# Kernel tuning notes

Measured on AMD Instinct MI355X. Metric: run time of the kernel, lower is better.

## Reference

```python
import jax, jax.numpy as jnp
import numpy as np

D_IN = 1024
D_OUT = 1024
SEQ = 2048
BATCH = 4


def setup_inputs() -> dict:
    key = jax.random.key(0)
    kx, kq, kk, kv = jax.random.split(key, 4)
    x = jax.random.normal(kx, (BATCH, SEQ, D_IN), dtype=jnp.float32)
    s = 1.0 / np.sqrt(D_IN)
    Wq = jax.random.uniform(kq, (D_IN, D_OUT), dtype=jnp.float32, minval=-s, maxval=s)
    Wk = jax.random.uniform(kk, (D_IN, D_OUT), dtype=jnp.float32, minval=-s, maxval=s)
    Wv = jax.random.uniform(kv, (D_IN, D_OUT), dtype=jnp.float32, minval=-s, maxval=s)
    return {"x": x, "Wq": Wq, "Wk": Wk, "Wv": Wv}


def reference(x, Wq, Wk, Wv):
    d_k = Wq.shape[1]
    q = jnp.einsum('bsd,de->bse', x, Wq)
    k = jnp.einsum('bsd,de->bse', x, Wk)
    v = jnp.einsum('bsd,de->bse', x, Wv)
    # [B, S, S] raw scores
    scores = jnp.einsum('bqe,bke->bqk', q, k)
    S = scores.shape[-1]
    causal = jnp.triu(jnp.ones((S, S), dtype=bool), k=1)  # True above diagonal
    scores = jnp.where(causal, -jnp.inf, scores)
    attn = jax.nn.softmax(scores * (d_k ** -0.5), axis=-1)
    # dropout p=0.0 -> identity
    return jnp.einsum('bqk,bke->bqe', attn, v)
```

## Files before the change

### kernel.cpp

```cpp
#include <hip/hip_runtime.h>
#include <hip/hip_bf16.h>

typedef unsigned short u16;
typedef __bf16 bfx8 __attribute__((ext_vector_type(8)));
typedef float fx4 __attribute__((ext_vector_type(4)));

#define SEQ 2048
#define DIM 1024
#define NBATCH 4
#define SCALE 0.03125f
#define NEL ((size_t)NBATCH * SEQ * DIM)

__device__ inline u16 f2bf(float f) {
    __bf16 h = (__bf16)f;
    return __builtin_bit_cast(unsigned short, h);
}

#define GLL(gp, lp) __builtin_amdgcn_global_load_lds( \
    (const __attribute__((address_space(1))) unsigned int*)(gp), \
    (__attribute__((address_space(3))) unsigned int*)(lp), 16, 0, 0)

__global__ __launch_bounds__(256) void prep(
    const float* __restrict__ X,
    const float* __restrict__ Wq, const float* __restrict__ Wk,
    const float* __restrict__ Wv,
    u16* __restrict__ XB, u16* __restrict__ WT, float* __restrict__ Lrow)
{
    __shared__ u16 t[32][33];
    int bid = blockIdx.x;
    int tid = threadIdx.x;
    if (bid < 8192) {
        size_t i = (size_t)bid * 256 + tid;
        float4 v = ((const float4*)X)[i];
        uint2 pk;
        pk.x = (unsigned)f2bf(v.x) | ((unsigned)f2bf(v.y) << 16);
        pk.y = (unsigned)f2bf(v.z) | ((unsigned)f2bf(v.w) << 16);
        ((uint2*)XB)[i] = pk;
    } else if (bid < 11264) {
        int tt = bid - 8192;
        int z = tt >> 10, t2 = tt & 1023;
        const float* W = (z == 0) ? Wq : (z == 1) ? Wk : Wv;
        u16* out = WT + (size_t)z * 1024 * 1024;
        int n0 = (t2 & 31) * 32, k0 = (t2 >> 5) * 32;
        int tx = tid & 31, ty = tid >> 5;
        #pragma unroll
        for (int i = 0; i < 32; i += 8)
            t[ty + i][tx] = f2bf(W[(size_t)(k0 + ty + i) * 1024 + n0 + tx]);
        __syncthreads();
        #pragma unroll
        for (int i = 0; i < 32; i += 8)
            out[(size_t)(n0 + ty + i) * 1024 + k0 + tx] = t[tx][ty + i];
    } else {
        int i = (bid - 11264) * 256 + tid;
        Lrow[i] = 0.0f;
    }
}

__global__ __launch_bounds__(256) void gemm_fast(
    const u16* __restrict__ XB, const u16* __restrict__ WT,
    u16* __restrict__ Qo, u16* __restrict__ Ko, u16* __restrict__ VTo)
{
    const u16* Wz = WT + (size_t)blockIdx.z * 1024 * 1024;
    int m0 = blockIdx.y * 128, n0 = blockIdx.x * 128;

    __shared__ __align__(16) u16 As[128 * 32];
    __shared__ __align__(16) u16 Bs[128 * 32];
    __shared__ __align__(16) u16 Ct[64][132];

    int tid = threadIdx.x, lane = tid & 63, w = tid >> 6;
    int wm = w >> 1, wn = w & 1, lo = lane & 15, qd = lane >> 4;

    fx4 acc[4][4] = {};

    int c0 = tid, c1 = tid + 256;
    const u16* a0 = XB + (size_t)(m0 + (c0 >> 2)) * 1024 + (c0 & 3) * 8;
    const u16* a1 = XB + (size_t)(m0 + (c1 >> 2)) * 1024 + (c1 & 3) * 8;
    const u16* b0 = Wz + (size_t)(n0 + (c0 >> 2)) * 1024 + (c0 & 3) * 8;
    const u16* b1 = Wz + (size_t)(n0 + (c1 >> 2)) * 1024 + (c1 & 3) * 8;

    for (int k0 = 0; k0 < 1024; k0 += 32) {
        GLL(a0 + k0, &As[(size_t)c0 * 8]);
        GLL(a1 + k0, &As[(size_t)c1 * 8]);
        GLL(b0 + k0, &Bs[(size_t)c0 * 8]);
        GLL(b1 + k0, &Bs[(size_t)c1 * 8]);
        __syncthreads();

        bfx8 af[4], bf[4];
        #pragma unroll
        for (int i = 0; i < 4; i++)
            af[i] = *(const bfx8*)(&As[(wm * 64 + i * 16 + lo) * 32 + qd * 8]);
        #pragma unroll
        for (int j = 0; j < 4; j++)
            bf[j] = *(const bfx8*)(&Bs[(wn * 64 + j * 16 + lo) * 32 + qd * 8]);
        #pragma unroll
        for (int i = 0; i < 4; i++)
            #pragma unroll
            for (int j = 0; j < 4; j++)
                acc[i][j] = __builtin_amdgcn_mfma_f32_16x16x32_bf16(af[i], bf[j], acc[i][j], 0, 0, 0);
        __syncthreads();
    }

    if (blockIdx.z != 2) {
        u16* C = (blockIdx.z == 0) ? Qo : Ko;
        #pragma unroll
        for (int i = 0; i < 4; i++)
            #pragma unroll
            for (int j = 0; j < 4; j++)
                #pragma unroll
                for (int r = 0; r < 4; r++) {
                    int row = m0 + wm * 64 + i * 16 + qd * 4 + r;
                    int col = n0 + wn * 64 + j * 16 + lo;
                    C[(size_t)row * 1024 + col] = f2bf(acc[i][j][r]);
                }
    } else {
        #pragma unroll
        for (int half = 0; half < 2; half++) {
            __syncthreads();
            if (wm == half) {
                #pragma unroll
                for (int i = 0; i < 4; i++)
                    #pragma unroll
                    for (int j = 0; j < 4; j++)
                        #pragma unroll
                        for (int r = 0; r < 4; r++)
                            Ct[i * 16 + qd * 4 + r][wn * 64 + j * 16 + lo] = f2bf(acc[i][j][r]);
            }
            __syncthreads();
            #pragma unroll
            for (int e = tid; e < 64 * 128; e += 256) {
                int d = e >> 6, sl = e & 63;
                int gr = m0 + half * 64 + sl;
                int bb = gr >> 11, s = gr & 2047;
                VTo[((size_t)bb * DIM + (n0 + d)) * SEQ + s] = Ct[sl][d];
            }
        }
    }
}

__global__ __launch_bounds__(256) void gemm_legacy(
    const float* __restrict__ X,
    const float* __restrict__ Wq, const float* __restrict__ Wk, const float* __restrict__ Wv,
    u16* __restrict__ Qo, u16* __restrict__ Ko, u16* __restrict__ VTo)
{
    const int K = 1024, N = 1024;
    const float* W = (blockIdx.z == 0) ? Wq : (blockIdx.z == 1) ? Wk : Wv;
    int m0 = blockIdx.y * 128, n0 = blockIdx.x * 128;
    __shared__ __align__(16) u16 As[128 * 40];
    __shared__ __align__(16) u16 Bs[128 * 40];
    __shared__ __align__(16) u16 Ct[64][132];
    int tid = threadIdx.x, lane = tid & 63, w = tid >> 6;
    int wm = w >> 1, wn = w & 1, lo = lane & 15, qd = lane >> 4;
    fx4 acc[4][4] = {};
    for (int k0 = 0; k0 < K; k0 += 32) {
        #pragma unroll
        for (int c = tid; c < 1024; c += 256) {
            int row = c >> 3, cc = (c & 7) * 4;
            float4 v = *(const float4*)(X + (size_t)(m0 + row) * K + k0 + cc);
            uint2 pk;
            pk.x = (unsigned)f2bf(v.x) | ((unsigned)f2bf(v.y) << 16);
            pk.y = (unsigned)f2bf(v.z) | ((unsigned)f2bf(v.w) << 16);
            *(uint2*)(&As[row * 40 + cc]) = pk;
        }
        #pragma unroll
        for (int c = tid; c < 1024; c += 256) {
            int r = c >> 5, cc = (c & 31) * 4;
            float4 v = *(const float4*)(W + (size_t)(k0 + r) * N + n0 + cc);
            Bs[(cc + 0) * 40 + r] = f2bf(v.x);
            Bs[(cc + 1) * 40 + r] = f2bf(v.y);
            Bs[(cc + 2) * 40 + r] = f2bf(v.z);
            Bs[(cc + 3) * 40 + r] = f2bf(v.w);
        }
        __syncthreads();
        bfx8 af[4], bf[4];
        #pragma unroll
        for (int i = 0; i < 4; i++)
            af[i] = *(const bfx8*)(&As[(wm * 64 + i * 16 + lo) * 40 + qd * 8]);
        #pragma unroll
        for (int j = 0; j < 4; j++)
            bf[j] = *(const bfx8*)(&Bs[(wn * 64 + j * 16 + lo) * 40 + qd * 8]);
        #pragma unroll
        for (int i = 0; i < 4; i++)
            #pragma unroll
            for (int j = 0; j < 4; j++)
                acc[i][j] = __builtin_amdgcn_mfma_f32_16x16x32_bf16(af[i], bf[j], acc[i][j], 0, 0, 0);
        __syncthreads();
    }
    if (blockIdx.z != 2) {
        u16* C = (blockIdx.z == 0) ? Qo : Ko;
        #pragma unroll
        for (int i = 0; i < 4; i++)
            #pragma unroll
            for (int j = 0; j < 4; j++)
                #pragma unroll
                for (int r = 0; r < 4; r++) {
                    int row = m0 + wm * 64 + i * 16 + qd * 4 + r;
                    int col = n0 + wn * 64 + j * 16 + lo;
                    C[(size_t)row * N + col] = f2bf(acc[i][j][r]);
                }
    } else {
        #pragma unroll
        for (int half = 0; half < 2; half++) {
            __syncthreads();
            if (wm == half) {
                #pragma unroll
                for (int i = 0; i < 4; i++)
                    #pragma unroll
                    for (int j = 0; j < 4; j++)
                        #pragma unroll
                        for (int r = 0; r < 4; r++)
                            Ct[i * 16 + qd * 4 + r][wn * 64 + j * 16 + lo] = f2bf(acc[i][j][r]);
            }
            __syncthreads();
            #pragma unroll
            for (int e = tid; e < 64 * 128; e += 256) {
                int d = e >> 6, sl = e & 63;
                int gr = m0 + half * 64 + sl;
                int bb = gr >> 11, s = gr & 2047;
                VTo[((size_t)bb * DIM + (n0 + d)) * SEQ + s] = Ct[sl][d];
            }
        }
    }
}

__global__ __launch_bounds__(512) void sgemm_exp(
    const u16* __restrict__ Q, const u16* __restrict__ K,
    u16* __restrict__ P, float* __restrict__ Lrow)
{
    int b = blockIdx.y;
    int t = blockIdx.x;
    int i = (int)((sqrtf(8.0f * t + 1.0f) - 1.0f) * 0.5f);
    while ((i + 1) * (i + 2) / 2 <= t) i++;
    while (i * (i + 1) / 2 > t) i--;
    int j = t - i * (i + 1) / 2;

    const u16* Qb = Q + (size_t)b * SEQ * DIM;
    const u16* Kb = K + (size_t)b * SEQ * DIM;
    u16* Pb = P + (size_t)b * SEQ * SEQ;
    float* Lb = Lrow + (size_t)b * SEQ;

    int m0 = i * 128, n0 = j * 128;

    __shared__ __align__(16) u16 As[128 * 32];
    __shared__ __align__(16) u16 Bs[128 * 32];

    int tid = threadIdx.x, lane = tid & 63, w = tid >> 6;
    int wm = w >> 2, wn = w & 3, lo = lane & 15, qd = lane >> 4;

    fx4 acc[4][2] = {};

    int c0 = tid;
    const u16* a0 = Qb + (size_t)(m0 + (c0 >> 2)) * DIM + (c0 & 3) * 8;
    const u16* b0 = Kb + (size_t)(n0 + (c0 >> 2)) * DIM + (c0 & 3) * 8;

    for (int k0 = 0; k0 < 1024; k0 += 32) {
        GLL(a0 + k0, &As[(size_t)c0 * 8]);
        GLL(b0 + k0, &Bs[(size_t)c0 * 8]);
        __syncthreads();

        bfx8 af[4], bf[2];
        #pragma unroll
        for (int ii = 0; ii < 4; ii++)
            af[ii] = *(const bfx8*)(&As[(wm * 64 + ii * 16 + lo) * 32 + qd * 8]);
        #pragma unroll
        for (int jn = 0; jn < 2; jn++)
            bf[jn] = *(const bfx8*)(&Bs[(wn * 32 + jn * 16 + lo) * 32 + qd * 8]);
        #pragma unroll
        for (int ii = 0; ii < 4; ii++)
            #pragma unroll
            for (int jn = 0; jn < 2; jn++)
                acc[ii][jn] = __builtin_amdgcn_mfma_f32_16x16x32_bf16(af[ii], bf[jn], acc[ii][jn], 0, 0, 0);
        __syncthreads();
    }

    #pragma unroll
    for (int ii = 0; ii < 4; ii++)
        #pragma unroll
        for (int r = 0; r < 4; r++) {
            int row = m0 + wm * 64 + ii * 16 + qd * 4 + r;
            float rs = 0.0f;
            #pragma unroll
            for (int jn = 0; jn < 2; jn++) {
                int col = n0 + wn * 32 + jn * 16 + lo;
                float s = acc[ii][jn][r] * SCALE;
                s = fminf(fmaxf(s, -30.0f), 30.0f);
                float p = (col > row) ? 0.0f : __expf(s);
                Pb[(size_t)row * SEQ + col] = f2bf(p);
                rs += p;
            }
            #pragma unroll
            for (int off = 1; off < 16; off <<= 1) rs += __shfl_xor(rs, off);
            if (lo == 0) atomicAdd(&Lb[row], rs);
        }
}

__global__ __launch_bounds__(512) void pvgemm(
    const u16* __restrict__ P, const u16* __restrict__ VT,
    const float* __restrict__ Lrow, float* __restrict__ O)
{
    int b = blockIdx.y;
    int qb = 15 - (int)(blockIdx.x >> 3);
    int db = blockIdx.x & 7;
    int m0 = qb * 128, n0 = db * 128;
    int kext = (qb + 1) * 128;

    const u16* Pb = P + (size_t)b * SEQ * SEQ;
    const u16* Vb = VT + (size_t)b * DIM * SEQ;
    const float* Lb = Lrow + (size_t)b * SEQ;
    float* Ob = O + (size_t)b * SEQ * DIM;

    __shared__ __align__(16) u16 As[128 * 32];
    __shared__ __align__(16) u16 Bs[128 * 32];

    int tid = threadIdx.x, lane = tid & 63, w = tid >> 6;
    int wm = w >> 2, wn = w & 3, lo = lane & 15, qd = lane >> 4;

    fx4 acc[4][2] = {};

    int c0 = tid;
    const u16* a0 = Pb + (size_t)(m0 + (c0 >> 2)) * SEQ + (c0 & 3) * 8;
    const u16* b0 = Vb + (size_t)(n0 + (c0 >> 2)) * SEQ + (c0 & 3) * 8;

    for (int k0 = 0; k0 < kext; k0 += 32) {
        GLL(a0 + k0, &As[(size_t)c0 * 8]);
        GLL(b0 + k0, &Bs[(size_t)c0 * 8]);
        __syncthreads();

        bfx8 af[4], bf[2];
        #pragma unroll
        for (int ii = 0; ii < 4; ii++)
            af[ii] = *(const bfx8*)(&As[(wm * 64 + ii * 16 + lo) * 32 + qd * 8]);
        #pragma unroll
        for (int jn = 0; jn < 2; jn++)
            bf[jn] = *(const bfx8*)(&Bs[(wn * 32 + jn * 16 + lo) * 32 + qd * 8]);
        #pragma unroll
        for (int ii = 0; ii < 4; ii++)
            #pragma unroll
            for (int jn = 0; jn < 2; jn++)
                acc[ii][jn] = __builtin_amdgcn_mfma_f32_16x16x32_bf16(af[ii], bf[jn], acc[ii][jn], 0, 0, 0);
        __syncthreads();
    }

    #pragma unroll
    for (int ii = 0; ii < 4; ii++)
        #pragma unroll
        for (int r = 0; r < 4; r++) {
            int row = m0 + wm * 64 + ii * 16 + qd * 4 + r;
            float linv = 1.0f / Lb[row];
            #pragma unroll
            for (int jn = 0; jn < 2; jn++) {
                int col = n0 + wn * 32 + jn * 16 + lo;
                Ob[(size_t)row * DIM + col] = acc[ii][jn][r] * linv;
            }
        }
}

__global__ __launch_bounds__(512) void flash_attn(
    const u16* __restrict__ Q, const u16* __restrict__ Kmat,
    const u16* __restrict__ VT, float* __restrict__ O)
{
    int b = blockIdx.y;
    int qt = (int)(gridDim.x - 1) - (int)blockIdx.x;
    int q0 = qt * 32;
    int tid = threadIdx.x;
    int lane = tid & 63, w = tid >> 6;
    int lo = lane & 15, qd = lane >> 4;

    __shared__ __align__(16) float Sp[8][32][33];
    __shared__ __align__(16) __bf16 Pl[32][40];
    __shared__ float ml[32], ll[32], al[32];

    const u16* Qb = Q + (size_t)b * SEQ * DIM;
    const u16* Kb = Kmat + (size_t)b * SEQ * DIM;
    const u16* VTb = VT + (size_t)b * DIM * SEQ;

    bfx8 qf[2][4];
    #pragma unroll
    for (int i = 0; i < 2; i++)
        #pragma unroll
        for (int c = 0; c < 4; c++)
            qf[i][c] = *(const bfx8*)(Qb + (size_t)(q0 + i * 16 + lo) * DIM + w * 128 + c * 32 + qd * 8);

    fx4 oacc[2][8] = {};
    if (tid < 32) { ml[tid] = -INFINITY; ll[tid] = 0.0f; }
    __syncthreads();

    for (int kt = 0; kt <= qt; kt++) {
        int k0 = kt * 32;
        fx4 sp[2][2] = {};
        #pragma unroll
        for (int c = 0; c < 4; c++) {
            bfx8 kf[2];
            #pragma unroll
            for (int jn = 0; jn < 2; jn++)
                kf[jn] = *(const bfx8*)(Kb + (size_t)(k0 + jn * 16 + lo) * DIM + w * 128 + c * 32 + qd * 8);
            #pragma unroll
            for (int i = 0; i < 2; i++)
                #pragma unroll
                for (int jn = 0; jn < 2; jn++)
                    sp[i][jn] = __builtin_amdgcn_mfma_f32_16x16x32_bf16(qf[i][c], kf[jn], sp[i][jn], 0, 0, 0);
        }
        #pragma unroll
        for (int i = 0; i < 2; i++)
            #pragma unroll
            for (int jn = 0; jn < 2; jn++)
                #pragma unroll
                for (int r = 0; r < 4; r++)
                    Sp[w][i * 16 + qd * 4 + r][jn * 16 + lo] = sp[i][jn][r];
        __syncthreads();
        {
            int r = tid >> 4, ci = tid & 15;
            int q = q0 + r;
            float s0 = 0.0f, s1 = 0.0f;
            #pragma unroll
            for (int p = 0; p < 8; p++) { s0 += Sp[p][r][ci]; s1 += Sp[p][r][ci + 16]; }
            s0 = fminf(fmaxf(s0 * SCALE, -1e30f), 1e30f);
            s1 = fminf(fmaxf(s1 * SCALE, -1e30f), 1e30f);
            if (k0 + ci > q)      s0 = -INFINITY;
            if (k0 + ci + 16 > q) s1 = -INFINITY;
            float mx = fmaxf(s0, s1);
            #pragma unroll
            for (int off = 1; off < 16; off <<= 1) mx = fmaxf(mx, __shfl_xor(mx, off));
            float mo = ml[r];
            float mn = fmaxf(mo, mx);
            float p0 = __expf(s0 - mn), p1 = __expf(s1 - mn);
            Pl[r][ci] = (__bf16)p0;
            Pl[r][ci + 16] = (__bf16)p1;
            float ps = p0 + p1;
            #pragma unroll
            for (int off = 1; off < 16; off <<= 1) ps += __shfl_xor(ps, off);
            if (ci == 0) {
                float alpha = __expf(mo - mn);
                ll[r] = alpha * ll[r] + ps;
                ml[r] = mn;
                al[r] = alpha;
            }
        }
        __syncthreads();
        float alocal[2][4];
        #pragma unroll
        for (int i = 0; i < 2; i++)
            #pragma unroll
            for (int r = 0; r < 4; r++)
                alocal[i][r] = al[i * 16 + qd * 4 + r];
        #pragma unroll
        for (int i = 0; i < 2; i++)
            #pragma unroll
            for (int j = 0; j < 8; j++)
                #pragma unroll
                for (int r = 0; r < 4; r++)
                    oacc[i][j][r] *= alocal[i][r];
        bfx8 pf[2];
        #pragma unroll
        for (int i = 0; i < 2; i++)
            pf[i] = *(const bfx8*)(&Pl[i * 16 + lo][qd * 8]);
        #pragma unroll
        for (int j = 0; j < 8; j++) {
            bfx8 vf = *(const bfx8*)(VTb + (size_t)(w * 128 + j * 16 + lo) * SEQ + k0 + qd * 8);
            #pragma unroll
            for (int i = 0; i < 2; i++)
                oacc[i][j] = __builtin_amdgcn_mfma_f32_16x16x32_bf16(pf[i], vf, oacc[i][j], 0, 0, 0);
        }
    }

    float linv[2][4];
    #pragma unroll
    for (int i = 0; i < 2; i++)
        #pragma unroll
        for (int r = 0; r < 4; r++)
            linv[i][r] = 1.0f / ll[i * 16 + qd * 4 + r];
    float* Ob = O + (size_t)b * SEQ * DIM;
    #pragma unroll
    for (int i = 0; i < 2; i++)
        #pragma unroll
        for (int j = 0; j < 8; j++)
            #pragma unroll
            for (int r = 0; r < 4; r++) {
                int row = q0 + i * 16 + qd * 4 + r;
                int col = w * 128 + j * 16 + lo;
                Ob[(size_t)row * DIM + col] = oacc[i][j][r] * linv[i][r];
            }
}

extern "C" void kernel_launch(void* const* d_in, const int* in_sizes, int n_in,
                              void* d_out, int out_size, void* d_ws, size_t ws_size,
                              hipStream_t stream) {
    const float* x  = (const float*)d_in[0];
    const float* Wq = (const float*)d_in[1];
    const float* Wk = (const float*)d_in[2];
    const float* Wv = (const float*)d_in[3];

    u16* ws = (u16*)d_ws;
    u16* Qp  = ws;
    u16* Kp  = Qp + NEL;
    u16* VTp = Kp + NEL;
    u16* XBp = VTp + NEL;
    u16* WTp = XBp + NEL;
    u16*   Pm   = VTp + NEL;
    float* Lrow = (float*)(Pm + (size_t)NBATCH * SEQ * SEQ);

    size_t need_base = 3 * NEL * 2;
    size_t need_conv = NEL * 2 + (size_t)3 * 1024 * 1024 * 2;
    size_t need_mat  = (size_t)NBATCH * SEQ * SEQ * 2
                     + (size_t)NBATCH * SEQ * 4 + 1024;
    bool fastg = ws_size >= need_base + need_conv;
    bool mat   = ws_size >= need_base + need_mat;

    if (fastg && mat) {
        prep<<<dim3(11296), 256, 0, stream>>>(x, Wq, Wk, Wv, XBp, WTp, Lrow);
        gemm_fast<<<dim3(8, 64, 3), 256, 0, stream>>>(XBp, WTp, Qp, Kp, VTp);
        sgemm_exp<<<dim3(136, NBATCH), 512, 0, stream>>>(Qp, Kp, Pm, Lrow);
        pvgemm<<<dim3(128, NBATCH), 512, 0, stream>>>(Pm, VTp, Lrow, (float*)d_out);
    } else {
        gemm_legacy<<<dim3(8, 64, 3), 256, 0, stream>>>(x, Wq, Wk, Wv, Qp, Kp, VTp);
        flash_attn<<<dim3(SEQ / 32, NBATCH), 512, 0, stream>>>(
            Qp, Kp, VTp, (float*)d_out);
    }
}
```

Before: 255.1 us.

## Fold Wq·Wkᵀ into one matrix, swizzle LDS, and widen K-tiles

```diff
diff --git a/kernel.cpp b/kernel.cpp
--- a/kernel.cpp
+++ b/kernel.cpp
@@ -24,7 +24,8 @@
     const float* __restrict__ X,
     const float* __restrict__ Wq, const float* __restrict__ Wk,
     const float* __restrict__ Wv,
-    u16* __restrict__ XB, u16* __restrict__ WT, float* __restrict__ Lrow)
+    u16* __restrict__ XB, u16* __restrict__ WB, u16* __restrict__ WTv,
+    float* __restrict__ Lrow)
 {
     __shared__ u16 t[32][33];
     int bid = blockIdx.x;
@@ -36,62 +37,63 @@
         pk.x = (unsigned)f2bf(v.x) | ((unsigned)f2bf(v.y) << 16);
         pk.y = (unsigned)f2bf(v.z) | ((unsigned)f2bf(v.w) << 16);
         ((uint2*)XB)[i] = pk;
+    } else if (bid < 10240) {
+        int b2 = bid - 8192;
+        const float* W = (b2 < 1024) ? Wq : Wk;
+        u16* out = WB + (size_t)(b2 >> 10) * 1024 * 1024;
+        size_t i = (size_t)(b2 & 1023) * 256 + tid;
+        float4 v = ((const float4*)W)[i];
+        uint2 pk;
+        pk.x = (unsigned)f2bf(v.x) | ((unsigned)f2bf(v.y) << 16);
+        pk.y = (unsigned)f2bf(v.z) | ((unsigned)f2bf(v.w) << 16);
+        ((uint2*)out)[i] = pk;
     } else if (bid < 11264) {
-        int tt = bid - 8192;
-        int z = tt >> 10, t2 = tt & 1023;
-        const float* W = (z == 0) ? Wq : (z == 1) ? Wk : Wv;
-        u16* out = WT + (size_t)z * 1024 * 1024;
+        int t2 = bid - 10240;
         int n0 = (t2 & 31) * 32, k0 = (t2 >> 5) * 32;
         int tx = tid & 31, ty = tid >> 5;
         #pragma unroll
         for (int i = 0; i < 32; i += 8)
-            t[ty + i][tx] = f2bf(W[(size_t)(k0 + ty + i) * 1024 + n0 + tx]);
+            t[ty + i][tx] = f2bf(Wv[(size_t)(k0 + ty + i) * 1024 + n0 + tx]);
         __syncthreads();
         #pragma unroll
         for (int i = 0; i < 32; i += 8)
-            out[(size_t)(n0 + ty + i) * 1024 + k0 + tx] = t[tx][ty + i];
+            WTv[(size_t)(n0 + ty + i) * 1024 + k0 + tx] = t[tx][ty + i];
     } else {
         int i = (bid - 11264) * 256 + tid;
         Lrow[i] = 0.0f;
     }
 }
 
-__global__ __launch_bounds__(256) void gemm_fast(
-    const u16* __restrict__ XB, const u16* __restrict__ WT,
-    u16* __restrict__ Qo, u16* __restrict__ Ko, u16* __restrict__ VTo)
-{
-    const u16* Wz = WT + (size_t)blockIdx.z * 1024 * 1024;
+__global__ __launch_bounds__(256) void gemm_m(
+    const u16* __restrict__ WBk, const u16* __restrict__ WBq, u16* __restrict__ MT)
+{
     int m0 = blockIdx.y * 128, n0 = blockIdx.x * 128;
-
     __shared__ __align__(16) u16 As[128 * 32];
     __shared__ __align__(16) u16 Bs[128 * 32];
-    __shared__ __align__(16) u16 Ct[64][132];
-
     int tid = threadIdx.x, lane = tid & 63, w = tid >> 6;
     int wm = w >> 1, wn = w & 1, lo = lane & 15, qd = lane >> 4;
-
     fx4 acc[4][4] = {};
 
     int c0 = tid, c1 = tid + 256;
-    const u16* a0 = XB + (size_t)(m0 + (c0 >> 2)) * 1024 + (c0 & 3) * 8;
-    const u16* a1 = XB + (size_t)(m0 + (c1 >> 2)) * 1024 + (c1 & 3) * 8;
-    const u16* b0 = Wz + (size_t)(n0 + (c0 >> 2)) * 1024 + (c0 & 3) * 8;
-    const u16* b1 = Wz + (size_t)(n0 + (c1 >> 2)) * 1024 + (c1 & 3) * 8;
-
+    const u16* a0 = WBk + (size_t)(m0 + (c0 >> 2)) * 1024 + (((c0 & 3) ^ ((c0 >> 2) & 3)) * 8);
+    const u16* a1 = WBk + (size_t)(m0 + (c1 >> 2)) * 1024 + (((c1 & 3) ^ ((c1 >> 2) & 3)) * 8);
+    const u16* b0 = WBq + (size_t)(n0 + (c0 >> 2)) * 1024 + (((c0 & 3) ^ ((c0 >> 2) & 3)) * 8);
+    const u16* b1 = WBq + (size_t)(n0 + (c1 >> 2)) * 1024 + (((c1 & 3) ^ ((c1 >> 2) & 3)) * 8);
+
+    int sw = (qd ^ (lo & 3)) * 8;
     for (int k0 = 0; k0 < 1024; k0 += 32) {
         GLL(a0 + k0, &As[(size_t)c0 * 8]);
         GLL(a1 + k0, &As[(size_t)c1 * 8]);
         GLL(b0 + k0, &Bs[(size_t)c0 * 8]);
         GLL(b1 + k0, &Bs[(size_t)c1 * 8]);
         __syncthreads();
-
         bfx8 af[4], bf[4];
         #pragma unroll
         for (int i = 0; i < 4; i++)
-            af[i] = *(const bfx8*)(&As[(wm * 64 + i * 16 + lo) * 32 + qd * 8]);
+            af[i] = *(const bfx8*)(&As[(wm * 64 + i * 16 + lo) * 32 + sw]);
         #pragma unroll
         for (int j = 0; j < 4; j++)
-            bf[j] = *(const bfx8*)(&Bs[(wn * 64 + j * 16 + lo) * 32 + qd * 8]);
+            bf[j] = *(const bfx8*)(&Bs[(wn * 64 + j * 16 + lo) * 32 + sw]);
         #pragma unroll
         for (int i = 0; i < 4; i++)
             #pragma unroll
@@ -99,9 +101,63 @@
                 acc[i][j] = __builtin_amdgcn_mfma_f32_16x16x32_bf16(af[i], bf[j], acc[i][j], 0, 0, 0);
         __syncthreads();
     }
-
-    if (blockIdx.z != 2) {
-        u16* C = (blockIdx.z == 0) ? Qo : Ko;
+    #pragma unroll
+    for (int i = 0; i < 4; i++)
+        #pragma unroll
+        for (int j = 0; j < 4; j++)
+            #pragma unroll
+            for (int r = 0; r < 4; r++)
+                MT[(size_t)(m0 + wm * 64 + i * 16 + qd * 4 + r) * 1024
+                   + n0 + wn * 64 + j * 16 + lo] = f2bf(acc[i][j][r]);
+}
+
+__global__ __launch_bounds__(256) void gemm_fast(
+    const u16* __restrict__ XB, const u16* __restrict__ MT,
+    const u16* __restrict__ WTv,
+    u16* __restrict__ Yo, u16* __restrict__ VTo)
+{
+    const u16* Wz = (blockIdx.z == 0) ? MT : WTv;
+    int m0 = blockIdx.y * 128, n0 = blockIdx.x * 128;
+
+    __shared__ __align__(16) u16 As[128 * 32];
+    __shared__ __align__(16) u16 Bs[128 * 32];
+    __shared__ __align__(16) u16 Ct[64][132];
+
+    int tid = threadIdx.x, lane = tid & 63, w = tid >> 6;
+    int wm = w >> 1, wn = w & 1, lo = lane & 15, qd = lane >> 4;
+
+    fx4 acc[4][4] = {};
+
+    int c0 = tid, c1 = tid + 256;
+    const u16* a0 = XB + (size_t)(m0 + (c0 >> 2)) * 1024 + (((c0 & 3) ^ ((c0 >> 2) & 3)) * 8);
+    const u16* a1 = XB + (size_t)(m0 + (c1 >> 2)) * 1024 + (((c1 & 3) ^ ((c1 >> 2) & 3)) * 8);
+    const u16* b0 = Wz + (size_t)(n0 + (c0 >> 2)) * 1024 + (((c0 & 3) ^ ((c0 >> 2) & 3)) * 8);
+    const u16* b1 = Wz + (size_t)(n0 + (c1 >> 2)) * 1024 + (((c1 & 3) ^ ((c1 >> 2) & 3)) * 8);
+
+    int sw = (qd ^ (lo & 3)) * 8;
+    for (int k0 = 0; k0 < 1024; k0 += 32) {
+        GLL(a0 + k0, &As[(size_t)c0 * 8]);
+        GLL(a1 + k0, &As[(size_t)c1 * 8]);
+        GLL(b0 + k0, &Bs[(size_t)c0 * 8]);
+        GLL(b1 + k0, &Bs[(size_t)c1 * 8]);
+        __syncthreads();
+
+        bfx8 af[4], bf[4];
+        #pragma unroll
+        for (int i = 0; i < 4; i++)
+            af[i] = *(const bfx8*)(&As[(wm * 64 + i * 16 + lo) * 32 + sw]);
+        #pragma unroll
+        for (int j = 0; j < 4; j++)
+            bf[j] = *(const bfx8*)(&Bs[(wn * 64 + j * 16 + lo) * 32 + sw]);
+        #pragma unroll
+        for (int i = 0; i < 4; i++)
+            #pragma unroll
+            for (int j = 0; j < 4; j++)
+                acc[i][j] = __builtin_amdgcn_mfma_f32_16x16x32_bf16(af[i], bf[j], acc[i][j], 0, 0, 0);
+        __syncthreads();
+    }
+
+    if (blockIdx.z == 0) {
         #pragma unroll
         for (int i = 0; i < 4; i++)
             #pragma unroll
@@ -110,7 +166,7 @@
                 for (int r = 0; r < 4; r++) {
                     int row = m0 + wm * 64 + i * 16 + qd * 4 + r;
                     int col = n0 + wn * 64 + j * 16 + lo;
-                    C[(size_t)row * 1024 + col] = f2bf(acc[i][j][r]);
+                    Yo[(size_t)row * 1024 + col] = f2bf(acc[i][j][r]);
                 }
     } else {
         #pragma unroll
@@ -135,6 +191,154 @@
             }
         }
     }
+}
+
+__global__ __launch_bounds__(512) void sgemm_exp(
+    const u16* __restrict__ Y, const u16* __restrict__ XB,
+    u16* __restrict__ P, float* __restrict__ Lrow)
+{
+    int b = blockIdx.y;
+    int t = blockIdx.x;
+    int i = (int)((sqrtf(8.0f * t + 1.0f) - 1.0f) * 0.5f);
+    while ((i + 1) * (i + 2) / 2 <= t) i++;
+    while (i * (i + 1) / 2 > t) i--;
+    int j = t - i * (i + 1) / 2;
+
+    const u16* Yb = Y + (size_t)b * SEQ * DIM;
+    const u16* Xb = XB + (size_t)b * SEQ * DIM;
+    u16* Pb = P + (size_t)b * SEQ * SEQ;
+    float* Lb = Lrow + (size_t)b * SEQ;
+
+    int m0 = i * 128, n0 = j * 128;
+
+    __shared__ __align__(16) u16 As[128 * 64];
+    __shared__ __align__(16) u16 Bs[128 * 64];
+
+    int tid = threadIdx.x, lane = tid & 63, w = tid >> 6;
+    int wm = w >> 2, wn = w & 3, lo = lane & 15, qd = lane >> 4;
+
+    fx4 acc[4][2] = {};
+
+    int c0 = tid, c1 = tid + 512;
+    const u16* a0 = Yb + (size_t)(m0 + (c0 >> 3)) * 1024 + (((c0 & 7) ^ ((c0 >> 3) & 7)) * 8);
+    const u16* a1 = Yb + (size_t)(m0 + (c1 >> 3)) * 1024 + (((c1 & 7) ^ ((c1 >> 3) & 7)) * 8);
+    const u16* b0 = Xb + (size_t)(n0 + (c0 >> 3)) * 1024 + (((c0 & 7) ^ ((c0 >> 3) & 7)) * 8);
+    const u16* b1 = Xb + (size_t)(n0 + (c1 >> 3)) * 1024 + (((c1 & 7) ^ ((c1 >> 3) & 7)) * 8);
+
+    for (int k0 = 0; k0 < 1024; k0 += 64) {
+        GLL(a0 + k0, &As[(size_t)c0 * 8]);
+        GLL(a1 + k0, &As[(size_t)c1 * 8]);
+        GLL(b0 + k0, &Bs[(size_t)c0 * 8]);
+        GLL(b1 + k0, &Bs[(size_t)c1 * 8]);
+        __syncthreads();
+
+        #pragma unroll
+        for (int kc = 0; kc < 2; kc++) {
+            int sw = ((kc * 4 + qd) ^ (lo & 7)) * 8;
+            bfx8 af[4], bf[2];
+            #pragma unroll
+            for (int ii = 0; ii < 4; ii++)
+                af[ii] = *(const bfx8*)(&As[(wm * 64 + ii * 16 + lo) * 64 + sw]);
+            #pragma unroll
+            for (int jn = 0; jn < 2; jn++)
+                bf[jn] = *(const bfx8*)(&Bs[(wn * 32 + jn * 16 + lo) * 64 + sw]);
+            #pragma unroll
+            for (int ii = 0; ii < 4; ii++)
+                #pragma unroll
+                for (int jn = 0; jn < 2; jn++)
+                    acc[ii][jn] = __builtin_amdgcn_mfma_f32_16x16x32_bf16(af[ii], bf[jn], acc[ii][jn], 0, 0, 0);
+        }
+        __syncthreads();
+    }
+
+    #pragma unroll
+    for (int ii = 0; ii < 4; ii++)
+        #pragma unroll
+        for (int r = 0; r < 4; r++) {
+            int row = m0 + wm * 64 + ii * 16 + qd * 4 + r;
+            float rs = 0.0f;
+            #pragma unroll
+            for (int jn = 0; jn < 2; jn++) {
+                int col = n0 + wn * 32 + jn * 16 + lo;
+                float s = acc[ii][jn][r] * SCALE;
+                s = fminf(fmaxf(s, -30.0f), 30.0f);
+                float p = (col > row) ? 0.0f : __expf(s);
+                Pb[(size_t)row * SEQ + col] = f2bf(p);
+                rs += p;
+            }
+            #pragma unroll
+            for (int off = 1; off < 16; off <<= 1) rs += __shfl_xor(rs, off);
+            if (lo == 0) atomicAdd(&Lb[row], rs);
+        }
+}
+
+__global__ __launch_bounds__(512) void pvgemm(
+    const u16* __restrict__ P, const u16* __restrict__ VT,
+    const float* __restrict__ Lrow, float* __restrict__ O)
+{
+    int b = blockIdx.y;
+    int qb = 15 - (int)(blockIdx.x >> 3);
+    int db = blockIdx.x & 7;
+    int m0 = qb * 128, n0 = db * 128;
+    int kext = (qb + 1) * 128;
+
+    const u16* Pb = P + (size_t)b * SEQ * SEQ;
+    const u16* Vb = VT + (size_t)b * DIM * SEQ;
+    const float* Lb = Lrow + (size_t)b * SEQ;
+    float* Ob = O + (size_t)b * SEQ * DIM;
+
+    __shared__ __align__(16) u16 As[128 * 64];
+    __shared__ __align__(16) u16 Bs[128 * 64];
+
+    int tid = threadIdx.x, lane = tid & 63, w = tid >> 6;
+    int wm = w >> 2, wn = w & 3, lo = lane & 15, qd = lane >> 4;
+
+    fx4 acc[4][2] = {};
+
+    int c0 = tid, c1 = tid + 512;
+    const u16* a0 = Pb + (size_t)(m0 + (c0 >> 3)) * SEQ + (((c0 & 7) ^ ((c0 >> 3) & 7)) * 8);
+    const u16* a1 = Pb + (size_t)(m0 + (c1 >> 3)) * SEQ + (((c1 & 7) ^ ((c1 >> 3) & 7)) * 8);
+    const u16* b0 = Vb + (size_t)(n0 + (c0 >> 3)) * SEQ + (((c0 & 7) ^ ((c0 >> 3) & 7)) * 8);
+    const u16* b1 = Vb + (size_t)(n0 + (c1 >> 3)) * SEQ + (((c1 & 7) ^ ((c1 >> 3) & 7)) * 8);
+
+    for (int k0 = 0; k0 < kext; k0 += 64) {
+        GLL(a0 + k0, &As[(size_t)c0 * 8]);
+        GLL(a1 + k0, &As[(size_t)c1 * 8]);
+        GLL(b0 + k0, &Bs[(size_t)c0 * 8]);
+        GLL(b1 + k0, &Bs[(size_t)c1 * 8]);
+        __syncthreads();
+
+        #pragma unroll
+        for (int kc = 0; kc < 2; kc++) {
+            int sw = ((kc * 4 + qd) ^ (lo & 7)) * 8;
+            bfx8 af[4], bf[2];
+            #pragma unroll
+            for (int ii = 0; ii < 4; ii++)
+                af[ii] = *(const bfx8*)(&As[(wm * 64 + ii * 16 + lo) * 64 + sw]);
+            #pragma unroll
+            for (int jn = 0; jn < 2; jn++)
+                bf[jn] = *(const bfx8*)(&Bs[(wn * 32 + jn * 16 + lo) * 64 + sw]);
+            #pragma unroll
+            for (int ii = 0; ii < 4; ii++)
+                #pragma unroll
+                for (int jn = 0; jn < 2; jn++)
+                    acc[ii][jn] = __builtin_amdgcn_mfma_f32_16x16x32_bf16(af[ii], bf[jn], acc[ii][jn], 0, 0, 0);
+        }
+        __syncthreads();
+    }
+
+    #pragma unroll
+    for (int ii = 0; ii < 4; ii++)
+        #pragma unroll
+        for (int r = 0; r < 4; r++) {
+            int row = m0 + wm * 64 + ii * 16 + qd * 4 + r;
+            float linv = 1.0f / Lb[row];
+            #pragma unroll
+            for (int jn = 0; jn < 2; jn++) {
+                int col = n0 + wn * 32 + jn * 16 + lo;
+                Ob[(size_t)row * DIM + col] = acc[ii][jn][r] * linv;
+            }
+        }
 }
 
 __global__ __launch_bounds__(256) void gemm_legacy(
@@ -222,138 +426,6 @@
     }
 }
 
-__global__ __launch_bounds__(512) void sgemm_exp(
-    const u16* __restrict__ Q, const u16* __restrict__ K,
-    u16* __restrict__ P, float* __restrict__ Lrow)
-{
-    int b = blockIdx.y;
-    int t = blockIdx.x;
-    int i = (int)((sqrtf(8.0f * t + 1.0f) - 1.0f) * 0.5f);
-    while ((i + 1) * (i + 2) / 2 <= t) i++;
-    while (i * (i + 1) / 2 > t) i--;
-    int j = t - i * (i + 1) / 2;
-
-    const u16* Qb = Q + (size_t)b * SEQ * DIM;
-    const u16* Kb = K + (size_t)b * SEQ * DIM;
-    u16* Pb = P + (size_t)b * SEQ * SEQ;
-    float* Lb = Lrow + (size_t)b * SEQ;
-
-    int m0 = i * 128, n0 = j * 128;
-
-    __shared__ __align__(16) u16 As[128 * 32];
-    __shared__ __align__(16) u16 Bs[128 * 32];
-
-    int tid = threadIdx.x, lane = tid & 63, w = tid >> 6;
-    int wm = w >> 2, wn = w & 3, lo = lane & 15, qd = lane >> 4;
-
-    fx4 acc[4][2] = {};
-
-    int c0 = tid;
-    const u16* a0 = Qb + (size_t)(m0 + (c0 >> 2)) * DIM + (c0 & 3) * 8;
-    const u16* b0 = Kb + (size_t)(n0 + (c0 >> 2)) * DIM + (c0 & 3) * 8;
-
-    for (int k0 = 0; k0 < 1024; k0 += 32) {
-        GLL(a0 + k0, &As[(size_t)c0 * 8]);
-        GLL(b0 + k0, &Bs[(size_t)c0 * 8]);
-        __syncthreads();
-
-        bfx8 af[4], bf[2];
-        #pragma unroll
-        for (int ii = 0; ii < 4; ii++)
-            af[ii] = *(const bfx8*)(&As[(wm * 64 + ii * 16 + lo) * 32 + qd * 8]);
-        #pragma unroll
-        for (int jn = 0; jn < 2; jn++)
-            bf[jn] = *(const bfx8*)(&Bs[(wn * 32 + jn * 16 + lo) * 32 + qd * 8]);
-        #pragma unroll
-        for (int ii = 0; ii < 4; ii++)
-            #pragma unroll
-            for (int jn = 0; jn < 2; jn++)
-                acc[ii][jn] = __builtin_amdgcn_mfma_f32_16x16x32_bf16(af[ii], bf[jn], acc[ii][jn], 0, 0, 0);
-        __syncthreads();
-    }
-
-    #pragma unroll
-    for (int ii = 0; ii < 4; ii++)
-        #pragma unroll
-        for (int r = 0; r < 4; r++) {
-            int row = m0 + wm * 64 + ii * 16 + qd * 4 + r;
-            float rs = 0.0f;
-            #pragma unroll
-            for (int jn = 0; jn < 2; jn++) {
-                int col = n0 + wn * 32 + jn * 16 + lo;
-                float s = acc[ii][jn][r] * SCALE;
-                s = fminf(fmaxf(s, -30.0f), 30.0f);
-                float p = (col > row) ? 0.0f : __expf(s);
-                Pb[(size_t)row * SEQ + col] = f2bf(p);
-                rs += p;
-            }
-            #pragma unroll
-            for (int off = 1; off < 16; off <<= 1) rs += __shfl_xor(rs, off);
-            if (lo == 0) atomicAdd(&Lb[row], rs);
-        }
-}
-
-__global__ __launch_bounds__(512) void pvgemm(
-    const u16* __restrict__ P, const u16* __restrict__ VT,
-    const float* __restrict__ Lrow, float* __restrict__ O)
-{
-    int b = blockIdx.y;
-    int qb = 15 - (int)(blockIdx.x >> 3);
-    int db = blockIdx.x & 7;
-    int m0 = qb * 128, n0 = db * 128;
-    int kext = (qb + 1) * 128;
-
-    const u16* Pb = P + (size_t)b * SEQ * SEQ;
-    const u16* Vb = VT + (size_t)b * DIM * SEQ;
-    const float* Lb = Lrow + (size_t)b * SEQ;
-    float* Ob = O + (size_t)b * SEQ * DIM;
-
-    __shared__ __align__(16) u16 As[128 * 32];
-    __shared__ __align__(16) u16 Bs[128 * 32];
-
-    int tid = threadIdx.x, lane = tid & 63, w = tid >> 6;
-    int wm = w >> 2, wn = w & 3, lo = lane & 15, qd = lane >> 4;
-
-    fx4 acc[4][2] = {};
-
-    int c0 = tid;
-    const u16* a0 = Pb + (size_t)(m0 + (c0 >> 2)) * SEQ + (c0 & 3) * 8;
-    const u16* b0 = Vb + (size_t)(n0 + (c0 >> 2)) * SEQ + (c0 & 3) * 8;
-
-    for (int k0 = 0; k0 < kext; k0 += 32) {
-        GLL(a0 + k0, &As[(size_t)c0 * 8]);
-        GLL(b0 + k0, &Bs[(size_t)c0 * 8]);
-        __syncthreads();
-
-        bfx8 af[4], bf[2];
-        #pragma unroll
-        for (int ii = 0; ii < 4; ii++)
-            af[ii] = *(const bfx8*)(&As[(wm * 64 + ii * 16 + lo) * 32 + qd * 8]);
-        #pragma unroll
-        for (int jn = 0; jn < 2; jn++)
-            bf[jn] = *(const bfx8*)(&Bs[(wn * 32 + jn * 16 + lo) * 32 + qd * 8]);
-        #pragma unroll
-        for (int ii = 0; ii < 4; ii++)
-            #pragma unroll
-            for (int jn = 0; jn < 2; jn++)
-                acc[ii][jn] = __builtin_amdgcn_mfma_f32_16x16x32_bf16(af[ii], bf[jn], acc[ii][jn], 0, 0, 0);
-        __syncthreads();
-    }
-
-    #pragma unroll
-    for (int ii = 0; ii < 4; ii++)
-        #pragma unroll
-        for (int r = 0; r < 4; r++) {
-            int row = m0 + wm * 64 + ii * 16 + qd * 4 + r;
-            float linv = 1.0f / Lb[row];
-            #pragma unroll
-            for (int jn = 0; jn < 2; jn++) {
-                int col = n0 + wn * 32 + jn * 16 + lo;
-                Ob[(size_t)row * DIM + col] = acc[ii][jn][r] * linv;
-            }
-        }
-}
-
 __global__ __launch_bounds__(512) void flash_attn(
     const u16* __restrict__ Q, const u16* __restrict__ Kmat,
     const u16* __restrict__ VT, float* __restrict__ O)
@@ -490,29 +562,30 @@
     const float* Wv = (const float*)d_in[3];
 
     u16* ws = (u16*)d_ws;
-    u16* Qp  = ws;
-    u16* Kp  = Qp + NEL;
-    u16* VTp = Kp + NEL;
-    u16* XBp = VTp + NEL;
-    u16* WTp = XBp + NEL;
-    u16*   Pm   = VTp + NEL;
+    u16* Yp  = ws;
+    u16* VTp = ws + NEL;
+    u16* XBp = ws + 2 * NEL;
+    u16* WBp = ws + 3 * NEL;
+    u16* WTv = WBp + (size_t)2 * 1024 * 1024;
+    u16* MTp = WTv + (size_t)1024 * 1024;
+    u16* Pm  = MTp + (size_t)1024 * 1024;
     float* Lrow = (float*)(Pm + (size_t)NBATCH * SEQ * SEQ);
 
-    size_t need_base = 3 * NEL * 2;
-    size_t need_conv = NEL * 2 + (size_t)3 * 1024 * 1024 * 2;
-    size_t need_mat  = (size_t)NBATCH * SEQ * SEQ * 2
+    size_t need_mat = ((size_t)3 * NEL + (size_t)4 * 1024 * 1024
+                     + (size_t)NBATCH * SEQ * SEQ) * 2
                      + (size_t)NBATCH * SEQ * 4 + 1024;
-    bool fastg = ws_size >= need_base + need_conv;
-    bool mat   = ws_size >= need_base + need_mat;
-
-    if (fastg && mat) {
-        prep<<<dim3(11296), 256, 0, stream>>>(x, Wq, Wk, Wv, XBp, WTp, Lrow);
-        gemm_fast<<<dim3(8, 64, 3), 256, 0, stream>>>(XBp, WTp, Qp, Kp, VTp);
-        sgemm_exp<<<dim3(136, NBATCH), 512, 0, stream>>>(Qp, Kp, Pm, Lrow);
+
+    if (ws_size >= need_mat) {
+        prep<<<dim3(11296), 256, 0, stream>>>(x, Wq, Wk, Wv, XBp, WBp, WTv, Lrow);
+        gemm_m<<<dim3(8, 8), 256, 0, stream>>>(
+            WBp + (size_t)1024 * 1024 , WBp , MTp);
+        gemm_fast<<<dim3(8, 64, 2), 256, 0, stream>>>(XBp, MTp, WTv, Yp, VTp);
+        sgemm_exp<<<dim3(136, NBATCH), 512, 0, stream>>>(Yp, XBp, Pm, Lrow);
         pvgemm<<<dim3(128, NBATCH), 512, 0, stream>>>(Pm, VTp, Lrow, (float*)d_out);
     } else {
-        gemm_legacy<<<dim3(8, 64, 3), 256, 0, stream>>>(x, Wq, Wk, Wv, Qp, Kp, VTp);
+        u16* Qp = ws; u16* Kp = ws + NEL; u16* VTf = ws + 2 * NEL;
+        gemm_legacy<<<dim3(8, 64, 3), 256, 0, stream>>>(x, Wq, Wk, Wv, Qp, Kp, VTf);
         flash_attn<<<dim3(SEQ / 32, NBATCH), 512, 0, stream>>>(
-            Qp, Kp, VTp, (float*)d_out);
-    }
-}
+            Qp, Kp, VTf, (float*)d_out);
+    }
+}
```

Result: faster. 246.9 us (-3.2%).
